# Performance work log

Hardware: AMD Instinct MI355X
Metric: run time of the kernel (lower is better)

The kernel has to match this reference:

```python
import jax, jax.numpy as jnp
from jax import lax
import numpy as np

B, C_IN, H, W = 32, 128, 64, 64
C_OUT, K, KH, KW = 256, 4, 3, 3
HIDDEN = C_IN  # in_planes != 3 -> hidden_planes = in_planes
T_TEMP = 34.0
BN_EPS = 1e-5


def setup_inputs() -> dict:
    key = jax.random.key(0)
    ks = jax.random.split(key, 4)
    return {
        "x": jax.random.normal(ks[0], (B, C_IN, H, W), dtype=jnp.float32),
        "w_fc1": jax.random.normal(ks[1], (HIDDEN, C_IN), dtype=jnp.float32) * (2.0 / C_IN) ** 0.5,
        "bn1_gamma": jnp.ones((HIDDEN,), jnp.float32),
        "bn1_beta": jnp.zeros((HIDDEN,), jnp.float32),
        "bn1_mean": jnp.zeros((HIDDEN,), jnp.float32),
        "bn1_var": jnp.ones((HIDDEN,), jnp.float32),
        "w_fc2": jax.random.normal(ks[2], (K * C_IN, HIDDEN), dtype=jnp.float32) * (2.0 / HIDDEN) ** 0.5,
        "b_fc2": jnp.zeros((K * C_IN,), jnp.float32),
        "bn2_gamma": jnp.ones((K * C_IN,), jnp.float32),
        "bn2_beta": jnp.zeros((K * C_IN,), jnp.float32),
        "bn2_mean": jnp.zeros((K * C_IN,), jnp.float32),
        "bn2_var": jnp.ones((K * C_IN,), jnp.float32),
        "anchored_w": jax.random.normal(ks[3], (K, C_OUT, C_IN, KH, KW), dtype=jnp.float32) * (2.0 / (C_OUT * KH * KW)) ** 0.5,
        "anchored_b": jnp.zeros((K, C_OUT), jnp.float32),
    }


def _bn(v, gamma, beta, mean, var):
    return (v - mean) * gamma * lax.rsqrt(var + BN_EPS) + beta


def reference(x, w_fc1, bn1_gamma, bn1_beta, bn1_mean, bn1_var,
              w_fc2, b_fc2, bn2_gamma, bn2_beta, bn2_mean, bn2_var,
              anchored_w, anchored_b):
    # ----- CFG routing: squeeze-excite style softmax over K*C_in -----
    pooled = x.mean(axis=(2, 3))                      # [B, C_in]  (adaptive avg pool to 1x1)
    h = pooled @ w_fc1.T                              # [B, hidden] (1x1 conv, no bias)
    h = jax.nn.relu(_bn(h, bn1_gamma, bn1_beta, bn1_mean, bn1_var))
    t = h @ w_fc2.T + b_fc2                           # [B, K*C_in]
    t = _bn(t, bn2_gamma, bn2_beta, bn2_mean, bn2_var)
    theta = jax.nn.softmax(t / T_TEMP, axis=1)        # [B, K*C_in]
    theta_r = theta.reshape(-1, K, anchored_w.shape[2])  # [B, K, C_in]

    # ----- per-sample kernel mixture: sum_k theta[b,k,i] * W[k,o,i,h,w] -----
    w = jnp.einsum('bki,koihw->boihw', theta_r, anchored_w)  # [B, C_out, C_in, KH, KW]
    b = theta_r.mean(axis=2) @ anchored_b                    # [B, C_out]

    # ----- per-sample conv (equiv. to grouped conv with groups=B) -----
    def conv1(xi, wi):
        return lax.conv_general_dilated(
            xi[None], wi, window_strides=(1, 1), padding=((1, 1), (1, 1)),
            dimension_numbers=('NCHW', 'OIHW', 'NCHW'))[0]

    out = jax.vmap(conv1)(x, w) + b[:, :, None, None]  # [B, C_out, H, W]
    return out
```

## Files before the change

kernel.cpp:

```cpp
#include <hip/hip_runtime.h>
#include <hip/hip_bf16.h>

typedef __attribute__((ext_vector_type(8))) __bf16 bf16x8;
typedef __attribute__((ext_vector_type(4))) float f32x4;

__device__ __forceinline__ unsigned pk2bf(float lo, float hi) {
  __hip_bfloat162 h = __float22bfloat162_rn(make_float2(lo, hi));
  unsigned u;
  __builtin_memcpy(&u, &h, 4);
  return u;
}

__device__ __forceinline__ void gload_lds16(const void* g, void* l) {
  __builtin_amdgcn_global_load_lds(
      (const __attribute__((address_space(1))) unsigned int*)g,
      (__attribute__((address_space(3))) unsigned int*)l, 16, 0, 0);
}

__global__ __launch_bounds__(256) void k_pool_convert(
    const float* __restrict__ x, float* __restrict__ psum,
    unsigned short* __restrict__ xbf) {
  __shared__ float xs[128][65];
  const int b = blockIdx.x >> 6;
  const int y = blockIdx.x & 63;
  const int t = threadIdx.x;
  const float* src = x + ((size_t)b * 128) * 4096 + y * 64;
#pragma unroll
  for (int i = 0; i < 8; ++i) {
    int idx = t + i * 256;
    int c = idx >> 4, x4 = (idx & 15) << 2;
    float4 v = *(const float4*)(src + (size_t)c * 4096 + x4);
    xs[c][x4] = v.x; xs[c][x4 + 1] = v.y; xs[c][x4 + 2] = v.z; xs[c][x4 + 3] = v.w;
  }
  __syncthreads();
  if (t < 128) {
    float s = 0.f;
#pragma unroll
    for (int j = 0; j < 64; ++j) s += xs[t][j];
    psum[((size_t)b * 128 + t) * 64 + y] = s;
  }
#pragma unroll
  for (int i = 0; i < 4; ++i) {
    int idx = t + i * 256;
    int q = idx & 3, xx = (idx >> 2) & 63, g = idx >> 8;
    unsigned wd[4];
#pragma unroll
    for (int j = 0; j < 4; ++j)
      wd[j] = pk2bf(xs[g * 32 + q * 8 + 2 * j][xx], xs[g * 32 + q * 8 + 2 * j + 1][xx]);
    *(uint4*)(xbf + ((((size_t)b * 4 + g) * 4096) + y * 64 + xx) * 32 + q * 8) =
        make_uint4(wd[0], wd[1], wd[2], wd[3]);
  }
}

__global__ __launch_bounds__(128) void k_route(
    const float* __restrict__ psum, const float* __restrict__ w_fc1,
    const float* __restrict__ g1, const float* __restrict__ be1,
    const float* __restrict__ m1, const float* __restrict__ v1,
    const float* __restrict__ w_fc2, const float* __restrict__ bfc2,
    const float* __restrict__ g2, const float* __restrict__ be2,
    const float* __restrict__ m2, const float* __restrict__ v2,
    const float* __restrict__ ab, float* __restrict__ theta,
    float* __restrict__ bias) {
  __shared__ float pooled[128], hs[128], r2[8];
  const int b = blockIdx.x, t = threadIdx.x;
  const int wid = t >> 6;
  float s = 0.f;
  const float* ps = psum + ((size_t)b * 128 + t) * 64;
  for (int j = 0; j < 64; ++j) s += ps[j];
  pooled[t] = s * (1.0f / 4096.0f);
  __syncthreads();
  float acc = 0.f;
  const float* w1r = w_fc1 + t * 128;
  for (int i = 0; i < 128; ++i) acc += pooled[i] * w1r[i];
  acc = (acc - m1[t]) * g1[t] * rsqrtf(v1[t] + 1e-5f) + be1[t];
  hs[t] = fmaxf(acc, 0.f);
  __syncthreads();
  float tv[4];
  for (int q = 0; q < 4; ++q) {
    int m = q * 128 + t;
    const float* w2r = w_fc2 + (size_t)m * 128;
    float a2 = bfc2[m];
    for (int i = 0; i < 128; ++i) a2 += hs[i] * w2r[i];
    a2 = (a2 - m2[m]) * g2[m] * rsqrtf(v2[m] + 1e-5f) + be2[m];
    tv[q] = a2 * (1.0f / 34.0f);
  }
  float mx4 = fmaxf(fmaxf(tv[0], tv[1]), fmaxf(tv[2], tv[3]));
  for (int o = 32; o; o >>= 1) mx4 = fmaxf(mx4, __shfl_xor(mx4, o));
  if ((t & 63) == 0) r2[wid] = mx4;
  __syncthreads();
  float mx = fmaxf(r2[0], r2[1]);
  float e[4], ss = 0.f;
  for (int q = 0; q < 4; ++q) { e[q] = expf(tv[q] - mx); ss += e[q]; }
  for (int o = 32; o; o >>= 1) ss += __shfl_xor(ss, o);
  if ((t & 63) == 0) r2[2 + wid] = ss;
  __syncthreads();
  float inv = 1.0f / (r2[2] + r2[3]);
  float th[4], tk[4];
  for (int q = 0; q < 4; ++q) { th[q] = e[q] * inv; theta[b * 512 + q * 128 + t] = th[q]; }
  for (int q = 0; q < 4; ++q) {
    float v = th[q];
    for (int o = 32; o; o >>= 1) v += __shfl_xor(v, o);
    tk[q] = v;
  }
  __syncthreads();
  if ((t & 63) == 0)
    for (int q = 0; q < 4; ++q) r2[wid * 4 + q] = tk[q];
  __syncthreads();
  for (int o = t; o < 256; o += 128) {
    float bb = 0.f;
    for (int k = 0; k < 4; ++k) bb += (r2[k] + r2[4 + k]) * (1.0f / 128.0f) * ab[k * 256 + o];
    bias[b * 256 + o] = bb;
  }
}

__global__ __launch_bounds__(256) void k_mix(
    const float* __restrict__ aw, const float* __restrict__ theta,
    unsigned short* __restrict__ wmix) {
  __shared__ float aw_s[4][32][33];
  __shared__ float th_s[32][4][32];
  const int bx = blockIdx.x;
  const int oq = bx & 3, obl = (bx >> 2) & 1, ks = bx >> 3;
  const int g = ks / 9, tt = ks % 9;
  const int tid = threadIdx.x;
#pragma unroll
  for (int i = 0; i < 16; ++i) {
    int e = tid + i * 256;
    int i32 = e & 31, o32 = (e >> 5) & 31, k = e >> 10;
    aw_s[k][i32][o32] =
        aw[((size_t)((k * 256 + obl * 128 + oq * 32 + o32) * 128) + g * 32 + i32) * 9 + tt];
    int kb = (e >> 5) & 3, bb = e >> 7;
    th_s[bb][kb][i32] = theta[bb * 512 + kb * 128 + g * 32 + i32];
  }
  __syncthreads();
  for (int it = 0; it < 16; ++it) {
    int b = it * 2 + (tid >> 7);
    int u = tid & 127;
    int o32 = u >> 2, q = u & 3;
    unsigned wd[4];
#pragma unroll
    for (int jj = 0; jj < 4; ++jj) {
      int i0 = q * 8 + jj * 2, i1 = i0 + 1;
      float v0 = th_s[b][0][i0] * aw_s[0][i0][o32] + th_s[b][1][i0] * aw_s[1][i0][o32]
               + th_s[b][2][i0] * aw_s[2][i0][o32] + th_s[b][3][i0] * aw_s[3][i0][o32];
      float v1 = th_s[b][0][i1] * aw_s[0][i1][o32] + th_s[b][1][i1] * aw_s[1][i1][o32]
               + th_s[b][2][i1] * aw_s[2][i1][o32] + th_s[b][3][i1] * aw_s[3][i1][o32];
      wd[jj] = pk2bf(v0, v1);
    }
    unsigned A = (unsigned)(((oq * 32 + o32) * 32 + q * 8) * 2);
    unsigned P = A ^ ((A >> 2) & 0x70u);
    size_t tilebase = (((size_t)b * 36 + ks) * 2 + obl) * 8192;
    *(uint4*)((char*)wmix + tilebase + P) = make_uint4(wd[0], wd[1], wd[2], wd[3]);
  }
}

__global__ __launch_bounds__(256, 2) void k_conv(
    const unsigned short* __restrict__ xbf, const unsigned short* __restrict__ wmix,
    const float* __restrict__ bias, float* __restrict__ out) {
  __shared__ __align__(16) char xls[21120];
  __shared__ __align__(16) char wls[2][16384];
  const int bx = blockIdx.x;
  const int wgid = ((bx & 7) << 7) | (bx >> 3);
  const int b = wgid >> 5, pblk = wgid & 31;
  const int tid = threadIdx.x;
  const int lane = tid & 63, wv = tid >> 6;
  const int y0 = pblk << 1;
  const int l15 = lane & 15, l4 = lane >> 4;

  unsigned a_off0 = ((unsigned)(l15 * 64 + l4 * 16)) ^ ((unsigned)(l15 & 7) << 4);
  a_off0 += (unsigned)(wv * 4096);

  f32x4 acc[4][8] = {};

  const unsigned short* xsrc_b = xbf + (size_t)b * 4 * 4096 * 32;

  auto stageW = [&](int ks, int buf) {
    const char* wsrc = (const char*)wmix + (size_t)(b * 36 + ks) * 16384;
#pragma unroll
    for (int p = 0; p < 4; ++p)
      gload_lds16(wsrc + p * 4096 + wv * 1024 + lane * 16,
                  wls[buf] + p * 4096 + wv * 1024);
  };

  uint4 xr[5];
  auto loadX = [&](int g) {
    const unsigned short* xsrc = xsrc_b + (size_t)g * (4096 * 32);
#pragma unroll
    for (int i = 0; i < 5; ++i) {
      int e = tid + i * 256;
      if (e > 1055) e = 1055;
      int q = e & 3, rc = e >> 2, c = rc % 66, r = rc / 66;
      int yy = y0 - 1 + r, xx = c - 1;
      uint4 v = make_uint4(0u, 0u, 0u, 0u);
      if ((unsigned)yy < 64u && (unsigned)xx < 64u)
        v = *(const uint4*)(xsrc + (((size_t)yy << 6) + xx) * 32 + q * 8);
      xr[i] = v;
    }
  };
  auto writeX = [&]() {
#pragma unroll
    for (int i = 0; i < 5; ++i) {
      int e = tid + i * 256;
      if (e > 1055) e = 1055;
      int q = e & 3, rc = e >> 2, c = rc % 66, r = rc / 66;
      *(uint4*)(xls + (r * 66 + c) * 80 + q * 16) = xr[i];
    }
  };

  loadX(0);
  stageW(0, 0);
  writeX();
  asm volatile("s_waitcnt lgkmcnt(0)" ::: "memory");

#pragma unroll
  for (int ks = 0; ks < 36; ++ks) {
    const int g = ks / 9, t = ks % 9;
    if (t == 8 && g < 3) asm volatile("s_waitcnt vmcnt(5)" ::: "memory");
    else                 asm volatile("s_waitcnt vmcnt(0)" ::: "memory");
    __builtin_amdgcn_s_barrier();
    asm volatile("" ::: "memory");
    if (t == 0 && g > 0) {
      writeX();
      asm volatile("s_waitcnt lgkmcnt(0)" ::: "memory");
      __builtin_amdgcn_s_barrier();
      asm volatile("" ::: "memory");
    }
    if (ks + 1 < 36) stageW(ks + 1, (ks + 1) & 1);
    if (t == 7 && g < 3) loadX(g + 1);
    const int dy = t / 3, dx = t % 3;
    bf16x8 bfr[8];
    const char* bbase = xls + (dy * 66 + dx + l15) * 80 + l4 * 16;
#pragma unroll
    for (int pf = 0; pf < 4; ++pf) bfr[pf] = *(const bf16x8*)(bbase + pf * 1280);
#pragma unroll
    for (int pf = 0; pf < 4; ++pf) bfr[pf + 4] = *(const bf16x8*)(bbase + 5280 + pf * 1280);
    bf16x8 afr[4];
    const char* abase = wls[ks & 1] + a_off0;
#pragma unroll
    for (int of = 0; of < 4; ++of) afr[of] = *(const bf16x8*)(abase + of * 1024);
    __builtin_amdgcn_s_setprio(1);
#pragma unroll
    for (int of = 0; of < 4; ++of)
#pragma unroll
      for (int pf = 0; pf < 8; ++pf)
        acc[of][pf] = __builtin_amdgcn_mfma_f32_16x16x32_bf16(afr[of], bfr[pf], acc[of][pf], 0, 0, 0);
    __builtin_amdgcn_s_setprio(0);
  }

  const float* bp = bias + b * 256 + wv * 64;
  float bv[4][4];
#pragma unroll
  for (int of = 0; of < 4; ++of)
#pragma unroll
    for (int j = 0; j < 4; ++j) bv[of][j] = bp[of * 16 + l4 * 4 + j];
  size_t outbase = ((size_t)(b * 256 + wv * 64)) * 4096 + (size_t)y0 * 64;
#pragma unroll
  for (int of = 0; of < 4; ++of)
#pragma unroll
    for (int pf = 0; pf < 8; ++pf) {
      int py = pf >> 2, px0 = (pf & 3) * 16;
#pragma unroll
      for (int j = 0; j < 4; ++j)
        out[outbase + (size_t)(of * 16 + l4 * 4 + j) * 4096 + py * 64 + px0 + l15] =
            acc[of][pf][j] + bv[of][j];
    }
}

extern "C" void kernel_launch(void* const* d_in, const int* in_sizes, int n_in,
                              void* d_out, int out_size, void* d_ws, size_t ws_size,
                              hipStream_t stream) {
  const float* x     = (const float*)d_in[0];
  const float* w_fc1 = (const float*)d_in[1];
  const float* g1    = (const float*)d_in[2];
  const float* be1   = (const float*)d_in[3];
  const float* m1    = (const float*)d_in[4];
  const float* v1    = (const float*)d_in[5];
  const float* w_fc2 = (const float*)d_in[6];
  const float* bfc2  = (const float*)d_in[7];
  const float* g2    = (const float*)d_in[8];
  const float* be2   = (const float*)d_in[9];
  const float* m2    = (const float*)d_in[10];
  const float* v2    = (const float*)d_in[11];
  const float* aw    = (const float*)d_in[12];
  const float* ab    = (const float*)d_in[13];
  float* out = (float*)d_out;

  char* ws = (char*)d_ws;
  unsigned short* xbf  = (unsigned short*)(ws);
  unsigned short* wmix = (unsigned short*)(ws + 33554432);
  float* psum  = (float*)(ws + 52428800);
  float* theta = (float*)(ws + 53477376);
  float* bias  = (float*)(ws + 53542912);

  hipLaunchKernelGGL(k_pool_convert, dim3(2048), dim3(256), 0, stream, x, psum, xbf);
  hipLaunchKernelGGL(k_route, dim3(32), dim3(128), 0, stream, psum, w_fc1, g1, be1, m1, v1,
                     w_fc2, bfc2, g2, be2, m2, v2, ab, theta, bias);
  hipLaunchKernelGGL(k_mix, dim3(288), dim3(256), 0, stream, aw, theta, wmix);
  hipLaunchKernelGGL(k_conv, dim3(1024), dim3(256), 0, stream, xbf, wmix, bias, out);
}
```

Baseline: 139.0 us.

## Load mixed weight fragments directly into registers with a 3-deep prefetch ring

The mixing kernel now writes weights in a per-lane fragment order, so each conv wave can read its MFMA A operands straight from global memory into registers. This replaces the double-buffered LDS staging through global_load_lds. A three-slot register ring prefetches weights three k-steps ahead. Most per-step barriers and vmcnt waits are dropped, and the x halo load is reshaped to skip clamped duplicate loads. The cost is higher register pressure and exposed global-load latency if three steps of prefetch are not enough.

```diff
diff --git a/kernel.cpp b/kernel.cpp
--- a/kernel.cpp
+++ b/kernel.cpp
@@ -9,12 +9,6 @@
   unsigned u;
   __builtin_memcpy(&u, &h, 4);
   return u;
-}
-
-__device__ __forceinline__ void gload_lds16(const void* g, void* l) {
-  __builtin_amdgcn_global_load_lds(
-      (const __attribute__((address_space(1))) unsigned int*)g,
-      (__attribute__((address_space(3))) unsigned int*)l, 16, 0, 0);
 }
 
 __global__ __launch_bounds__(256) void k_pool_convert(
@@ -146,10 +140,10 @@
                + th_s[b][2][i1] * aw_s[2][i1][o32] + th_s[b][3][i1] * aw_s[3][i1][o32];
       wd[jj] = pk2bf(v0, v1);
     }
-    unsigned A = (unsigned)(((oq * 32 + o32) * 32 + q * 8) * 2);
-    unsigned P = A ^ ((A >> 2) & 0x70u);
-    size_t tilebase = (((size_t)b * 36 + ks) * 2 + obl) * 8192;
-    *(uint4*)((char*)wmix + tilebase + P) = make_uint4(wd[0], wd[1], wd[2], wd[3]);
+    int o = obl * 128 + oq * 32 + o32;
+    unsigned off = (unsigned)((o >> 6) * 4096 + ((o >> 4) & 3) * 1024 + q * 256 + (o & 15) * 16);
+    size_t tilebase = ((size_t)b * 36 + ks) * 16384;
+    *(uint4*)((char*)wmix + tilebase + off) = make_uint4(wd[0], wd[1], wd[2], wd[3]);
   }
 }
 
@@ -157,7 +151,6 @@
     const unsigned short* __restrict__ xbf, const unsigned short* __restrict__ wmix,
     const float* __restrict__ bias, float* __restrict__ out) {
   __shared__ __align__(16) char xls[21120];
-  __shared__ __align__(16) char wls[2][16384];
   const int bx = blockIdx.x;
   const int wgid = ((bx & 7) << 7) | (bx >> 3);
   const int b = wgid >> 5, pblk = wgid & 31;
@@ -166,28 +159,18 @@
   const int y0 = pblk << 1;
   const int l15 = lane & 15, l4 = lane >> 4;
 
-  unsigned a_off0 = ((unsigned)(l15 * 64 + l4 * 16)) ^ ((unsigned)(l15 & 7) << 4);
-  a_off0 += (unsigned)(wv * 4096);
-
   f32x4 acc[4][8] = {};
 
   const unsigned short* xsrc_b = xbf + (size_t)b * 4 * 4096 * 32;
-
-  auto stageW = [&](int ks, int buf) {
-    const char* wsrc = (const char*)wmix + (size_t)(b * 36 + ks) * 16384;
-#pragma unroll
-    for (int p = 0; p < 4; ++p)
-      gload_lds16(wsrc + p * 4096 + wv * 1024 + lane * 16,
-                  wls[buf] + p * 4096 + wv * 1024);
-  };
+  const char* wtile = (const char*)wmix + (size_t)(b * 36) * 16384 +
+                      (size_t)wv * 4096 + (size_t)lane * 16;
 
   uint4 xr[5];
   auto loadX = [&](int g) {
     const unsigned short* xsrc = xsrc_b + (size_t)g * (4096 * 32);
 #pragma unroll
-    for (int i = 0; i < 5; ++i) {
+    for (int i = 0; i < 4; ++i) {
       int e = tid + i * 256;
-      if (e > 1055) e = 1055;
       int q = e & 3, rc = e >> 2, c = rc % 66, r = rc / 66;
       int yy = y0 - 1 + r, xx = c - 1;
       uint4 v = make_uint4(0u, 0u, 0u, 0u);
@@ -195,37 +178,57 @@
         v = *(const uint4*)(xsrc + (((size_t)yy << 6) + xx) * 32 + q * 8);
       xr[i] = v;
     }
+    if (tid < 32) {
+      int e = tid + 1024;
+      int q = e & 3, rc = e >> 2, c = rc % 66, r = rc / 66;
+      int yy = y0 - 1 + r, xx = c - 1;
+      uint4 v = make_uint4(0u, 0u, 0u, 0u);
+      if ((unsigned)yy < 64u && (unsigned)xx < 64u)
+        v = *(const uint4*)(xsrc + (((size_t)yy << 6) + xx) * 32 + q * 8);
+      xr[4] = v;
+    }
   };
   auto writeX = [&]() {
 #pragma unroll
-    for (int i = 0; i < 5; ++i) {
+    for (int i = 0; i < 4; ++i) {
       int e = tid + i * 256;
-      if (e > 1055) e = 1055;
       int q = e & 3, rc = e >> 2, c = rc % 66, r = rc / 66;
       *(uint4*)(xls + (r * 66 + c) * 80 + q * 16) = xr[i];
     }
+    if (tid < 32) {
+      int e = tid + 1024;
+      int q = e & 3, rc = e >> 2, c = rc % 66, r = rc / 66;
+      *(uint4*)(xls + (r * 66 + c) * 80 + q * 16) = xr[4];
+    }
   };
 
   loadX(0);
-  stageW(0, 0);
   writeX();
   asm volatile("s_waitcnt lgkmcnt(0)" ::: "memory");
+  bf16x8 wf[3][4];
+#pragma unroll
+  for (int s = 0; s < 3; ++s)
+#pragma unroll
+    for (int of = 0; of < 4; ++of)
+      wf[s][of] = *(const bf16x8*)(wtile + (size_t)s * 16384 + of * 1024);
+  __builtin_amdgcn_s_barrier();
+  asm volatile("" ::: "memory");
 
 #pragma unroll
   for (int ks = 0; ks < 36; ++ks) {
     const int g = ks / 9, t = ks % 9;
-    if (t == 8 && g < 3) asm volatile("s_waitcnt vmcnt(5)" ::: "memory");
-    else                 asm volatile("s_waitcnt vmcnt(0)" ::: "memory");
-    __builtin_amdgcn_s_barrier();
-    asm volatile("" ::: "memory");
     if (t == 0 && g > 0) {
+      __builtin_amdgcn_s_barrier();
+      asm volatile("" ::: "memory");
       writeX();
       asm volatile("s_waitcnt lgkmcnt(0)" ::: "memory");
       __builtin_amdgcn_s_barrier();
       asm volatile("" ::: "memory");
-    }
-    if (ks + 1 < 36) stageW(ks + 1, (ks + 1) & 1);
-    if (t == 7 && g < 3) loadX(g + 1);
+    } else if (ks > 0) {
+      __builtin_amdgcn_s_barrier();
+      asm volatile("" ::: "memory");
+    }
+    if (t == 8 && g < 3) loadX(g + 1);
     const int dy = t / 3, dx = t % 3;
     bf16x8 bfr[8];
     const char* bbase = xls + (dy * 66 + dx + l15) * 80 + l4 * 16;
@@ -233,17 +236,19 @@
     for (int pf = 0; pf < 4; ++pf) bfr[pf] = *(const bf16x8*)(bbase + pf * 1280);
 #pragma unroll
     for (int pf = 0; pf < 4; ++pf) bfr[pf + 4] = *(const bf16x8*)(bbase + 5280 + pf * 1280);
-    bf16x8 afr[4];
-    const char* abase = wls[ks & 1] + a_off0;
-#pragma unroll
-    for (int of = 0; of < 4; ++of) afr[of] = *(const bf16x8*)(abase + of * 1024);
     __builtin_amdgcn_s_setprio(1);
 #pragma unroll
     for (int of = 0; of < 4; ++of)
 #pragma unroll
       for (int pf = 0; pf < 8; ++pf)
-        acc[of][pf] = __builtin_amdgcn_mfma_f32_16x16x32_bf16(afr[of], bfr[pf], acc[of][pf], 0, 0, 0);
+        acc[of][pf] = __builtin_amdgcn_mfma_f32_16x16x32_bf16(wf[ks % 3][of], bfr[pf],
+                                                              acc[of][pf], 0, 0, 0);
     __builtin_amdgcn_s_setprio(0);
+    if (ks + 3 < 36) {
+#pragma unroll
+      for (int of = 0; of < 4; ++of)
+        wf[ks % 3][of] = *(const bf16x8*)(wtile + (size_t)(ks + 3) * 16384 + of * 1024);
+    }
   }
 
   const float* bp = bias + b * 256 + wv * 64;
```

New measurement: 141.8 us. +2.0%, slower.

## Give each wave its own weight slice and drop per-step block barriers

Applied to the files above, without the earlier changes.

Each wave now stages into LDS only the 4 KB weight slice it later reads itself. This removes the workgroup barrier that ran on every one of the 36 K-steps and replaces it with per-wave vmcnt waits. Block barriers remain only around the shared input-tile rewrite. The next input-tile prefetch moves one step later and becomes a branchless clamped load, and the tail LDS write now uses only the threads that need it. The risk is a race on the double-buffered weight slot if a wave's earlier LDS reads have not finished before its async global-to-LDS writes land.

```diff
diff --git a/kernel.cpp b/kernel.cpp
--- a/kernel.cpp
+++ b/kernel.cpp
@@ -174,11 +174,11 @@
   const unsigned short* xsrc_b = xbf + (size_t)b * 4 * 4096 * 32;
 
   auto stageW = [&](int ks, int buf) {
-    const char* wsrc = (const char*)wmix + (size_t)(b * 36 + ks) * 16384;
+    const char* wsrc = (const char*)wmix + (size_t)(b * 36 + ks) * 16384 + (size_t)wv * 4096;
 #pragma unroll
     for (int p = 0; p < 4; ++p)
-      gload_lds16(wsrc + p * 4096 + wv * 1024 + lane * 16,
-                  wls[buf] + p * 4096 + wv * 1024);
+      gload_lds16(wsrc + p * 1024 + lane * 16,
+                  wls[buf] + wv * 4096 + p * 1024);
   };
 
   uint4 xr[5];
@@ -190,19 +190,24 @@
       if (e > 1055) e = 1055;
       int q = e & 3, rc = e >> 2, c = rc % 66, r = rc / 66;
       int yy = y0 - 1 + r, xx = c - 1;
-      uint4 v = make_uint4(0u, 0u, 0u, 0u);
-      if ((unsigned)yy < 64u && (unsigned)xx < 64u)
-        v = *(const uint4*)(xsrc + (((size_t)yy << 6) + xx) * 32 + q * 8);
+      bool valid = ((unsigned)yy < 64u) && ((unsigned)xx < 64u);
+      size_t off = valid ? ((((size_t)yy << 6) + xx) * 32 + q * 8) : 0;
+      uint4 v = *(const uint4*)(xsrc + off);
+      if (!valid) v = make_uint4(0u, 0u, 0u, 0u);
       xr[i] = v;
     }
   };
   auto writeX = [&]() {
 #pragma unroll
-    for (int i = 0; i < 5; ++i) {
+    for (int i = 0; i < 4; ++i) {
       int e = tid + i * 256;
-      if (e > 1055) e = 1055;
       int q = e & 3, rc = e >> 2, c = rc % 66, r = rc / 66;
       *(uint4*)(xls + (r * 66 + c) * 80 + q * 16) = xr[i];
+    }
+    if (tid < 32) {
+      int e = tid + 1024;
+      int q = e & 3, rc = e >> 2, c = rc % 66, r = rc / 66;
+      *(uint4*)(xls + (r * 66 + c) * 80 + q * 16) = xr[4];
     }
   };
 
@@ -210,30 +215,32 @@
   stageW(0, 0);
   writeX();
   asm volatile("s_waitcnt lgkmcnt(0)" ::: "memory");
+  __builtin_amdgcn_s_barrier();
+  asm volatile("" ::: "memory");
 
 #pragma unroll
   for (int ks = 0; ks < 36; ++ks) {
     const int g = ks / 9, t = ks % 9;
-    if (t == 8 && g < 3) asm volatile("s_waitcnt vmcnt(5)" ::: "memory");
-    else                 asm volatile("s_waitcnt vmcnt(0)" ::: "memory");
-    __builtin_amdgcn_s_barrier();
-    asm volatile("" ::: "memory");
     if (t == 0 && g > 0) {
+      __builtin_amdgcn_s_barrier();
+      asm volatile("" ::: "memory");
       writeX();
       asm volatile("s_waitcnt lgkmcnt(0)" ::: "memory");
       __builtin_amdgcn_s_barrier();
       asm volatile("" ::: "memory");
     }
+    if (t == 8 && g < 3) loadX(g + 1);
     if (ks + 1 < 36) stageW(ks + 1, (ks + 1) & 1);
-    if (t == 7 && g < 3) loadX(g + 1);
+    if (ks == 35)            { asm volatile("s_waitcnt vmcnt(0)" ::: "memory"); }
+    else if (t == 8 && g < 3){ asm volatile("s_waitcnt vmcnt(9)" ::: "memory"); }
+    else                     { asm volatile("s_waitcnt vmcnt(4)" ::: "memory"); }
     const int dy = t / 3, dx = t % 3;
-    bf16x8 bfr[8];
-    const char* bbase = xls + (dy * 66 + dx + l15) * 80 + l4 * 16;
+    bf16x8 bfr[8], afr[4];
+    const char* bbase = xls + ((0 + dy) * 66 + dx + l15) * 80 + l4 * 16;
 #pragma unroll
     for (int pf = 0; pf < 4; ++pf) bfr[pf] = *(const bf16x8*)(bbase + pf * 1280);
 #pragma unroll
     for (int pf = 0; pf < 4; ++pf) bfr[pf + 4] = *(const bf16x8*)(bbase + 5280 + pf * 1280);
-    bf16x8 afr[4];
     const char* abase = wls[ks & 1] + a_off0;
 #pragma unroll
     for (int of = 0; of < 4; ++of) afr[of] = *(const bf16x8*)(abase + of * 1024);
```

After: 137.0 us. About the same (-1.4%).
